# Kernel tuning notes

Hardware: AMD Instinct MI355X
Metric: run time of the kernel (lower is better)

Reference implementation:

```python
import jax, jax.numpy as jnp
import numpy as np

N = 30000   # fluid particles
E = 480000  # edges
F = 4       # fluidFeatures (in channels)
P = 8       # RBF basis size per dim (dims=[8], 1D)
LAYERS = [32, 64, 64, 2]


def hat_basis(x, n):
    # 'linear' RBF: hat functions on n evenly spaced centers in [-1, 1]
    centers = jnp.linspace(-1.0, 1.0, n, dtype=x.dtype)
    spacing = 2.0 / (n - 1)
    return jnp.maximum(0.0, 1.0 - jnp.abs(x[:, None] - centers[None, :]) / spacing)  # [E, n]


def rbf_conv(x, fi, fj, d, W, b, mask, n_nodes):
    # x: [N, Cin]; d: [E, 1] clamped; W: [P, Cin, Cout]; b: [Cout]
    phi = hat_basis(d[:, 0], W.shape[0])      # [E, P]
    xj = x[fj]                                 # gather source features [E, Cin]
    msg = jnp.zeros((xj.shape[0], W.shape[2]), dtype=x.dtype)
    for p in range(W.shape[0]):                # small fixed P=8 loop keeps memory O(E*Cout)
        msg = msg + phi[:, p, None] * (xj @ W[p])
    msg = jnp.where(mask[:, None], msg, 0.0)   # centerIgnore: drop self edges fi==fj
    out = jax.ops.segment_sum(msg, fi, num_segments=n_nodes)  # scatter-reduce to targets
    return out + b


def _xavier(key, shape_in, shape_out):
    lim = float(np.sqrt(6.0 / (shape_in + shape_out)))
    return jax.random.uniform(key, (shape_in, shape_out), jnp.float32, -lim, lim)


def setup_inputs() -> dict:
    key = jax.random.key(0)
    ks = jax.random.split(key, 16)
    fluidFeatures = jax.random.normal(ks[0], (N, F), jnp.float32)
    fi = jax.random.randint(ks[1], (E,), 0, N)
    fj = jax.random.randint(ks[2], (E,), 0, N)
    distances = jax.random.normal(ks[3], (E, 1), jnp.float32)
    # conv channels: 4->32, 64->64, 64->64, 64->2
    cio = [(F, 32), (2 * 32, 64), (64, 64), (64, 2)]
    inp = {"fluidFeatures": fluidFeatures, "fi": fi, "fj": fj, "distances": distances}
    for li, (ci, co) in enumerate(cio):
        inp[f"cW{li}"] = jax.random.normal(ks[4 + li], (P, ci, co), jnp.float32) * (1.0 / np.sqrt(P * ci))
        inp[f"cb{li}"] = jnp.zeros((co,), jnp.float32)
        inp[f"fW{li}"] = _xavier(ks[8 + li], ci, co)   # stored [in, out]
        inp[f"fb{li}"] = jnp.zeros((co,), jnp.float32)
    return inp


def reference(fluidFeatures, fi, fj, distances,
              cW0, cb0, fW0, fb0, cW1, cb1, fW1, fb1,
              cW2, cb2, fW2, fb2, cW3, cb3, fW3, fb3):
    n_nodes = fluidFeatures.shape[0]
    mask = fi != fj                     # centerIgnore (mask instead of filter: jit-safe)
    d = jnp.clip(distances, -1.0, 1.0)

    conv0 = rbf_conv(fluidFeatures, fi, fj, d, cW0, cb0, mask, n_nodes)  # [N, 32]
    lin0 = fluidFeatures @ fW0 + fb0                                      # [N, 32]
    ans = jnp.concatenate([lin0, conv0], axis=1)                          # [N, 64]

    # i = 1: features[0]=32 != features[1]=64 -> no residual
    ansc = jax.nn.relu(ans)
    ans = rbf_conv(ansc, fi, fj, d, cW1, cb1, mask, n_nodes) + (ansc @ fW1 + fb1)
    # i = 2: features[1]==features[2]==64 and shapes match -> residual
    ansc = jax.nn.relu(ans)
    ans = rbf_conv(ansc, fi, fj, d, cW2, cb2, mask, n_nodes) + (ansc @ fW2 + fb2) + ans
    # i = 3: 64 -> 2, no residual
    ansc = jax.nn.relu(ans)
    ans = rbf_conv(ansc, fi, fj, d, cW3, cb3, mask, n_nodes) + (ansc @ fW3 + fb3)

    return ans  # dim == 1 (dims=[8]) -> no /128
```

## Files before the change

kernel.cpp:

```cpp
#include <hip/hip_runtime.h>


#define CAP 48

typedef __attribute__((ext_vector_type(8))) short short8;
typedef __attribute__((ext_vector_type(4))) short short4v;
typedef __attribute__((ext_vector_type(4))) float f32x4;

__device__ __forceinline__ short bf16s(float f) {
  unsigned u = __float_as_uint(f);
  return (short)((u + 0x7FFF + ((u >> 16) & 1)) >> 16);
}
__device__ __forceinline__ float b2f(unsigned short s) {
  return __uint_as_float(((unsigned)s) << 16);
}
__device__ __forceinline__ unsigned pack2(float a, float b) {
  return (unsigned)(unsigned short)bf16s(a) | ((unsigned)(unsigned short)bf16s(b) << 16);
}

__global__ void fill_prep(const float* __restrict__ dist,
                          const int* __restrict__ fi, const int* __restrict__ fj,
                          int* __restrict__ cnt, int* __restrict__ jw, int nE,
                          const float* __restrict__ cW1, const float* __restrict__ fW1,
                          const float* __restrict__ cW2, const float* __restrict__ fW2,
                          short* __restrict__ wt1, short* __restrict__ wt2,
                          const float* __restrict__ X,
                          const float* __restrict__ cW0,
                          const float* __restrict__ fW0,
                          unsigned short* __restrict__ U0, int n,
                          int fillBlocks, int prepBlocks) {
  if ((int)blockIdx.x < fillBlocks) {
    int e = blockIdx.x * blockDim.x + threadIdx.x;
    if (e >= nE) return;
    int i = fi[e], j = fj[e];
    if (i == j) return;
    float d = fminf(1.0f, fmaxf(-1.0f, dist[e]));
    float u = (d + 1.0f) * 3.5f;
    int p = min((int)u, 6);
    float w0 = 1.0f - (u - (float)p);
    int wq = (int)(w0 * 16383.0f + 0.5f);
    int pos = atomicAdd(&cnt[i], 1);
    if (pos < CAP)
      jw[(size_t)i * CAP + pos] = j | (p << 15) | (wq << 18);
  } else if ((int)blockIdx.x < fillBlocks + prepBlocks) {
    int idx = ((int)blockIdx.x - fillBlocks) * blockDim.x + threadIdx.x;
    if (idx >= 2 * 576 * 64) return;
    int sel = idx / (576 * 64);
    int r = idx - sel * (576 * 64);
    int col = r >> 6, ch = r & 63;
    const float* cW = sel ? cW2 : cW1;
    const float* fW = sel ? fW2 : fW1;
    float v;
    if (col < 512) {
      int p = col >> 6, co = col & 63;
      v = cW[((size_t)p * 64 + ch) * 64 + co];
    } else {
      v = fW[(size_t)ch * 64 + (col - 512)];
    }
    (sel ? wt2 : wt1)[(size_t)col * 64 + ch] = bf16s(v);
  } else {
    int idx = ((int)blockIdx.x - fillBlocks - prepBlocks) * blockDim.x + threadIdx.x;
    if (idx >= n * 72) return;
    int i = idx / 72, g = idx - i * 72;
    float4 x = *(const float4*)(X + (size_t)i * 4);
    float xk[4] = {x.x, x.y, x.z, x.w};
    float s[4] = {0, 0, 0, 0};
    if (g < 64) {
      int p = g >> 3;
      int co = (g * 4) & 31;
      #pragma unroll
      for (int k = 0; k < 4; ++k) {
        const float* wr = cW0 + ((size_t)p * 4 + k) * 32 + co;
        #pragma unroll
        for (int c = 0; c < 4; ++c) s[c] = fmaf(xk[k], wr[c], s[c]);
      }
    } else {
      int co = (g - 64) * 4;
      #pragma unroll
      for (int k = 0; k < 4; ++k) {
        const float* wr = fW0 + (size_t)k * 32 + co;
        #pragma unroll
        for (int c = 0; c < 4; ++c) s[c] = fmaf(xk[k], wr[c], s[c]);
      }
    }
    uint2 pk = make_uint2(pack2(s[0], s[1]), pack2(s[2], s[3]));
    *(uint2*)(U0 + (size_t)i * 288 + g * 4) = pk;
  }
}

__device__ __forceinline__ void gemm_tail(const unsigned short* sXa, short* sUL,
                                          const short* __restrict__ WT,
                                          int w, int lane) {
  const int mrow = lane & 15;
  const int quad = lane >> 4;
  short8 b0 = *(const short8*)(sXa + mrow * 64 + quad * 8);
  short8 b1 = *(const short8*)(sXa + mrow * 64 + quad * 8 + 32);
  const short* A0 = WT + (size_t)(w * 16 + mrow) * 64 + quad * 8;
  const short* A1 = WT + (size_t)((w + 16) * 16 + mrow) * 64 + quad * 8;
  short8 a00 = *(const short8*)(A0);
  short8 a01 = *(const short8*)(A0 + 32);
  short8 a10 = *(const short8*)(A1);
  short8 a11 = *(const short8*)(A1 + 32);
  const bool has3 = (w < 4);
  short8 a20 = {0, 0, 0, 0, 0, 0, 0, 0};
  short8 a21 = {0, 0, 0, 0, 0, 0, 0, 0};
  if (has3) {
    const short* A2 = WT + (size_t)((w + 32) * 16 + mrow) * 64 + quad * 8;
    a20 = *(const short8*)(A2);
    a21 = *(const short8*)(A2 + 32);
  }
  __builtin_amdgcn_sched_barrier(0);
  f32x4 acc0 = {0, 0, 0, 0}, acc1 = {0, 0, 0, 0};
  acc0 = __builtin_amdgcn_mfma_f32_16x16x32_bf16(a00, b0, acc0, 0, 0, 0);
  acc0 = __builtin_amdgcn_mfma_f32_16x16x32_bf16(a01, b1, acc0, 0, 0, 0);
  acc1 = __builtin_amdgcn_mfma_f32_16x16x32_bf16(a10, b0, acc1, 0, 0, 0);
  acc1 = __builtin_amdgcn_mfma_f32_16x16x32_bf16(a11, b1, acc1, 0, 0, 0);
  short4v pk;
  #pragma unroll
  for (int r = 0; r < 4; ++r) pk[r] = bf16s(acc0[r]);
  *(short4v*)(sUL + mrow * 584 + w * 16 + quad * 4) = pk;
  #pragma unroll
  for (int r = 0; r < 4; ++r) pk[r] = bf16s(acc1[r]);
  *(short4v*)(sUL + mrow * 584 + (w + 16) * 16 + quad * 4) = pk;
  if (has3) {
    f32x4 acc2 = {0, 0, 0, 0};
    acc2 = __builtin_amdgcn_mfma_f32_16x16x32_bf16(a20, b0, acc2, 0, 0, 0);
    acc2 = __builtin_amdgcn_mfma_f32_16x16x32_bf16(a21, b1, acc2, 0, 0, 0);
    #pragma unroll
    for (int r = 0; r < 4; ++r) pk[r] = bf16s(acc2[r]);
    *(short4v*)(sUL + mrow * 584 + (w + 32) * 16 + quad * 4) = pk;
  }
}

__global__ __launch_bounds__(1024, 8) void layer0_gemm(
    const unsigned short* __restrict__ U0,
    const int* __restrict__ cnt, const int* __restrict__ jw,
    const float* __restrict__ cb0, const float* __restrict__ fb0,
    const short* __restrict__ WTul,
    unsigned short* __restrict__ UL, int n) {
  __shared__ __align__(16) unsigned short sXa[16 * 64];
  __shared__ __align__(16) short sUL[16 * 584];
  const int tid = threadIdx.x;
  const int w = tid >> 6;
  const int lane = tid & 63;
  const int grp = lane >> 5;
  const int gl = lane & 31;
  const int nodeBase = blockIdx.x * 16;
  const int i = nodeBase + w;
  const bool valid = (i < n);
  const int ic = valid ? i : 0;

  int rec = jw[(size_t)ic * CAP + (lane < CAP ? lane : 0)];
  const int m = valid ? min(cnt[ic], CAP) : 0;
  const int mc = m - 1;
  float accLo = 0.0f, accHi = 0.0f;
  const unsigned* __restrict__ u0W = (const unsigned*)U0;
  unsigned rA[8], rB[8];
  float wA[8], wB[8];
#define L0_LOAD(R, WS, Q0)                                                  \
  _Pragma("unroll")                                                         \
  for (int k = 0; k < 8; ++k) {                                             \
    int eA = (Q0) + 2 * k;                                                  \
    int vA = __builtin_amdgcn_readlane(rec, min(eA, mc));                   \
    int vB = __builtin_amdgcn_readlane(rec, min(eA + 1, mc));               \
    int v = grp ? vB : vA;                                                  \
    int j = v & 0x7FFF;                                                     \
    int p = (v >> 15) & 7;                                                  \
    float w0 = (float)((unsigned)v >> 18) * (1.0f / 16383.0f);              \
    float wgt = (gl < 16) ? w0 : (1.0f - w0);                               \
    WS[k] = (eA + grp < m) ? wgt : 0.0f;                                    \
    R[k] = u0W[(size_t)j * 144 + p * 16 + gl];                              \
  }
#define L0_FMA(R, WS)                                                       \
  _Pragma("unroll")                                                         \
  for (int k = 0; k < 8; ++k) {                                             \
    accLo = fmaf(WS[k], __uint_as_float(R[k] << 16), accLo);                \
    accHi = fmaf(WS[k], __uint_as_float(R[k] & 0xFFFF0000u), accHi);        \
  }
  if (m > 0) {
    L0_LOAD(rA, wA, 0);
    L0_LOAD(rB, wB, 16);
    __builtin_amdgcn_sched_barrier(0);
    L0_FMA(rA, wA);
    if (m > 16) {
      L0_FMA(rB, wB);
      for (int q0 = 32; q0 < m; q0 += 16) {
        L0_LOAD(rA, wA, q0);
        __builtin_amdgcn_sched_barrier(0);
        L0_FMA(rA, wA);
      }
    }
  }
#undef L0_LOAD
#undef L0_FMA
  accLo += __shfl_xor(accLo, 16, 64);
  accHi += __shfl_xor(accHi, 16, 64);
  accLo += __shfl_xor(accLo, 32, 64);
  accHi += __shfl_xor(accHi, 32, 64);
  if (lane < 16) {
    const int l = lane;
    float c0v = fmaxf(accLo + cb0[2 * l], 0.0f);
    float c1v = fmaxf(accHi + cb0[2 * l + 1], 0.0f);
    unsigned lr = ((const unsigned*)(U0 + (size_t)ic * 288 + 256))[l];
    float l0 = fmaxf(__uint_as_float(lr << 16) + fb0[2 * l], 0.0f);
    float l1 = fmaxf(__uint_as_float(lr & 0xFFFF0000u) + fb0[2 * l + 1], 0.0f);
    unsigned* row = (unsigned*)(sXa + w * 64);
    row[l] = pack2(l0, l1);
    row[16 + l] = pack2(c0v, c1v);
  }
  __syncthreads();

  gemm_tail(sXa, sUL, WTul, w, lane);
  __syncthreads();
  const int r = tid >> 6;
  const int c0 = tid & 63;
  if (nodeBase + r < n) {
    unsigned short* dst = UL + (size_t)(nodeBase + r) * 576;
    #pragma unroll
    for (int chunk = c0; chunk < 72; chunk += 64)
      *(short8*)(dst + chunk * 8) = *(const short8*)(sUL + r * 584 + chunk * 8);
  }
}

__global__ __launch_bounds__(1024, 8) void conv_gemm(
    const unsigned short* __restrict__ ULA,
    const int* __restrict__ cnt, const int* __restrict__ jw,
    const float* __restrict__ cb, const float* __restrict__ fb,
    const short* __restrict__ WTul2,
    float* __restrict__ outAns,
    unsigned short* __restrict__ ULB, int n) {
  __shared__ __align__(16) unsigned short sXa[16 * 64];
  __shared__ __align__(16) short sUL[16 * 584];
  const int tid = threadIdx.x;
  const int w = tid >> 6;
  const int lane = tid & 63;
  const int half = lane >> 5;
  const int pl = lane & 31;
  const int nodeBase = blockIdx.x * 16;
  const int i = nodeBase + w;
  const bool valid = (i < n);
  const int ic = valid ? i : 0;

  int rec = jw[(size_t)ic * CAP + (lane < CAP ? lane : 0)];
  const int m = valid ? min(cnt[ic], CAP) : 0;
  const int mc = m - 1;
  const unsigned Lraw = ((const unsigned*)(ULA + (size_t)ic * 576 + 512))[pl];
  float accLo = 0.0f, accHi = 0.0f;
  const unsigned* __restrict__ ulaW = (const unsigned*)ULA;
  unsigned rA[16], rB[16];
#define C1_LOAD(R, Q0)                                                      \
  _Pragma("unroll")                                                         \
  for (int k = 0; k < 16; ++k) {                                            \
    int v = __builtin_amdgcn_readlane(rec, min((Q0) + k, mc));              \
    int j = v & 0x7FFF;                                                     \
    int p = (v >> 15) & 7;                                                  \
    R[k] = ulaW[(size_t)j * 288 + p * 32 + lane];                           \
  }
#define C1_FMA(R, Q0)                                                       \
  _Pragma("unroll")                                                         \
  for (int k = 0; k < 16; ++k) {                                            \
    int v = __builtin_amdgcn_readlane(rec, min((Q0) + k, mc));              \
    float w0 = (float)((unsigned)v >> 18) * (1.0f / 16383.0f);              \
    float wv = half ? (1.0f - w0) : w0;                                     \
    wv = ((Q0) + k < m) ? wv : 0.0f;                                        \
    accLo = fmaf(wv, __uint_as_float(R[k] << 16), accLo);                   \
    accHi = fmaf(wv, __uint_as_float(R[k] & 0xFFFF0000u), accHi);           \
  }
  if (m > 0) {
    C1_LOAD(rA, 0);
    C1_LOAD(rB, 16);
    __builtin_amdgcn_sched_barrier(0);
    C1_FMA(rA, 0);
    if (m > 16) {
      C1_FMA(rB, 16);
      for (int q0 = 32; q0 < m; q0 += 16) {
        C1_LOAD(rA, q0);
        __builtin_amdgcn_sched_barrier(0);
        C1_FMA(rA, q0);
      }
    }
  }
#undef C1_LOAD
#undef C1_FMA
  accLo += __shfl_xor(accLo, 32, 64);
  accHi += __shfl_xor(accHi, 32, 64);
  if (half == 0) {
    unsigned* row = (unsigned*)(sXa + w * 64);
    if (valid) {
      const int c0i = 2 * pl, c1i = c0i + 1;
      float o0 = accLo + __uint_as_float(Lraw << 16) + cb[c0i] + fb[c0i];
      float o1 = accHi + __uint_as_float(Lraw & 0xFFFF0000u) + cb[c1i] + fb[c1i];
      *(float2*)(outAns + (size_t)i * 64 + c0i) = make_float2(o0, o1);
      row[pl] = pack2(fmaxf(o0, 0.0f), fmaxf(o1, 0.0f));
    } else {
      row[pl] = 0u;
    }
  }
  __syncthreads();

  gemm_tail(sXa, sUL, WTul2, w, lane);
  __syncthreads();
  const int r = tid >> 6;
  const int c0 = tid & 63;
  if (nodeBase + r < n) {
    unsigned short* dst = ULB + (size_t)(nodeBase + r) * 576;
    #pragma unroll
    for (int chunk = c0; chunk < 72; chunk += 64)
      *(short8*)(dst + chunk * 8) = *(const short8*)(sUL + r * 584 + chunk * 8);
  }
}

__global__ __launch_bounds__(256, 8) void conv2_kernel(
    const unsigned short* __restrict__ UL,
    const int* __restrict__ cnt, const int* __restrict__ jw,
    const float* __restrict__ cb, const float* __restrict__ fb,
    const float* __restrict__ resid,
    const float* __restrict__ cW3,
    float* __restrict__ T,
    unsigned short* __restrict__ outAnsc, int n) {
  const int lane = threadIdx.x & 63;
  const int half = lane >> 5;
  const int pl = lane & 31;
  const int i = (blockIdx.x * blockDim.x + threadIdx.x) >> 6;
  if (i >= n) return;
  int rec = jw[(size_t)i * CAP + (lane < CAP ? lane : 0)];
  const int m = min(cnt[i], CAP);
  const int mc = m - 1;
  const unsigned Lraw = ((const unsigned*)(UL + (size_t)i * 576 + 512))[pl];
  float2 rv = *(const float2*)(resid + (size_t)i * 64 + 2 * pl);
  float accLo = 0.0f, accHi = 0.0f;
  const unsigned* __restrict__ ulW = (const unsigned*)UL;
  unsigned rA[16], rB[16];
#define C2_LOAD(R, Q0)                                                      \
  _Pragma("unroll")                                                         \
  for (int k = 0; k < 16; ++k) {                                            \
    int v = __builtin_amdgcn_readlane(rec, min((Q0) + k, mc));              \
    int j = v & 0x7FFF;                                                     \
    int p = (v >> 15) & 7;                                                  \
    R[k] = ulW[(size_t)j * 288 + p * 32 + lane];                            \
  }
#define C2_FMA(R, Q0)                                                       \
  _Pragma("unroll")                                                         \
  for (int k = 0; k < 16; ++k) {                                            \
    int v = __builtin_amdgcn_readlane(rec, min((Q0) + k, mc));              \
    float w0 = (float)((unsigned)v >> 18) * (1.0f / 16383.0f);              \
    float wv = half ? (1.0f - w0) : w0;                                     \
    wv = ((Q0) + k < m) ? wv : 0.0f;                                        \
    accLo = fmaf(wv, __uint_as_float(R[k] << 16), accLo);                   \
    accHi = fmaf(wv, __uint_as_float(R[k] & 0xFFFF0000u), accHi);           \
  }
  if (m > 0) {
    C2_LOAD(rA, 0);
    C2_LOAD(rB, 16);
    __builtin_amdgcn_sched_barrier(0);
    C2_FMA(rA, 0);
    if (m > 16) {
      C2_FMA(rB, 16);
      for (int q0 = 32; q0 < m; q0 += 16) {
        C2_LOAD(rA, q0);
        __builtin_amdgcn_sched_barrier(0);
        C2_FMA(rA, q0);
      }
    }
  }
#undef C2_LOAD
#undef C2_FMA
  accLo += __shfl_xor(accLo, 32, 64);
  accHi += __shfl_xor(accHi, 32, 64);
  if (half == 0) {
    const int c0i = 2 * pl, c1i = c0i + 1;
    float o0 = accLo + __uint_as_float(Lraw << 16) + cb[c0i] + fb[c0i] + rv.x;
    float o1 = accHi + __uint_as_float(Lraw & 0xFFFF0000u) + cb[c1i] + fb[c1i] + rv.y;
    unsigned short xb0 = (unsigned short)bf16s(fmaxf(o0, 0.0f));
    unsigned short xb1 = (unsigned short)bf16s(fmaxf(o1, 0.0f));
    ((unsigned*)(outAnsc + (size_t)i * 64))[pl] = (unsigned)xb0 | ((unsigned)xb1 << 16);
    float x0 = b2f(xb0), x1 = b2f(xb1);
    float c[16];
    #pragma unroll
    for (int t = 0; t < 16; ++t) {
      const float* wrow = cW3 + ((size_t)(t >> 1) * 64) * 2 + (t & 1);
      c[t] = x0 * wrow[c0i * 2] + x1 * wrow[c1i * 2];
    }
    #pragma unroll
    for (int off = 16; off > 0; off >>= 1) {
      #pragma unroll
      for (int t = 0; t < 16; ++t) c[t] += __shfl_xor(c[t], off, 64);
    }
    if (pl == 0) {
      float* tr = T + (size_t)i * 16;
      #pragma unroll
      for (int t = 0; t < 16; ++t) tr[t] = c[t];
    }
  }
}

__global__ __launch_bounds__(256, 4) void layer3_kernel(
    const unsigned short* __restrict__ Xb,
    const float* __restrict__ T,
    const int* __restrict__ cnt, const int* __restrict__ jw,
    const float* __restrict__ cb3, const float* __restrict__ fb3,
    const float* __restrict__ fW3,
    float* __restrict__ out, int n) {
  const int lane = threadIdx.x & 63;
  const int i = (blockIdx.x * blockDim.x + threadIdx.x) >> 6;
  if (i >= n) return;
  const int m = min(cnt[i], CAP);
  float c0 = 0.0f, c1 = 0.0f;
  if (lane < m) {
    int v = jw[(size_t)i * CAP + lane];
    int j = min(v & 0x7FFF, n - 1);
    int p = (v >> 15) & 7;
    float w0 = (float)((unsigned)v >> 18) * (1.0f / 16383.0f);
    float w1 = 1.0f - w0;
    const float* tb = T + (size_t)j * 16 + p * 2;
    float2 ta = *(const float2*)(tb);
    float2 tc = *(const float2*)(tb + 2);
    c0 = w0 * ta.x + w1 * tc.x;
    c1 = w0 * ta.y + w1 * tc.y;
  }
  float xi = b2f(Xb[(size_t)i * 64 + lane]);
  float2 fw = *(const float2*)(fW3 + lane * 2);
  c0 = fmaf(xi, fw.x, c0);
  c1 = fmaf(xi, fw.y, c1);
  #pragma unroll
  for (int off = 32; off > 0; off >>= 1) {
    c0 += __shfl_xor(c0, off, 64);
    c1 += __shfl_xor(c1, off, 64);
  }
  if (lane == 0) {
    out[(size_t)i * 2 + 0] = c0 + cb3[0] + fb3[0];
    out[(size_t)i * 2 + 1] = c1 + cb3[1] + fb3[1];
  }
}

extern "C" void kernel_launch(void* const* d_in, const int* in_sizes, int n_in,
                              void* d_out, int out_size, void* d_ws, size_t ws_size,
                              hipStream_t stream) {
  const float* X    = (const float*)d_in[0];
  const int*   fi   = (const int*)d_in[1];
  const int*   fj   = (const int*)d_in[2];
  const float* dist = (const float*)d_in[3];
  const float* cW0 = (const float*)d_in[4];  const float* cb0 = (const float*)d_in[5];
  const float* fW0 = (const float*)d_in[6];  const float* fb0 = (const float*)d_in[7];
  const float* cW1 = (const float*)d_in[8];  const float* cb1 = (const float*)d_in[9];
  const float* fW1 = (const float*)d_in[10]; const float* fb1 = (const float*)d_in[11];
  const float* cW2 = (const float*)d_in[12]; const float* cb2 = (const float*)d_in[13];
  const float* fW2 = (const float*)d_in[14]; const float* fb2 = (const float*)d_in[15];
  const float* cW3 = (const float*)d_in[16]; const float* cb3 = (const float*)d_in[17];
  const float* fW3 = (const float*)d_in[18]; const float* fb3 = (const float*)d_in[19];
  float* out = (float*)d_out;

  const int n  = in_sizes[0] / 4;
  const int nE = in_sizes[1];

  unsigned short* ULA   = (unsigned short*)d_ws;
  unsigned short* ULB   = ULA + (size_t)n * 576;
  unsigned short* U0    = ULB;
  float*          ans1  = (float*)(ULB + (size_t)n * 576);
  unsigned short* ansc2 = (unsigned short*)(ans1 + (size_t)n * 64);
  float* T     = (float*)(ansc2 + (size_t)n * 64);
  short* wtul1 = (short*)(T + (size_t)n * 16);
  short* wtul2 = wtul1 + 576 * 64;
  int*   jw    = (int*)(wtul2 + 576 * 64);
  int*   cnt   = jw + (size_t)n * CAP;

  hipMemsetAsync(cnt, 0, (size_t)n * sizeof(int), stream);
  const int fillBlocks = (nE + 255) / 256;
  const int prepBlocks = (2 * 576 * 64 + 255) / 256;
  const int u0Blocks   = (n * 72 + 255) / 256;
  fill_prep<<<fillBlocks + prepBlocks + u0Blocks, 256, 0, stream>>>(
      dist, fi, fj, cnt, jw, nE, cW1, fW1, cW2, fW2, wtul1, wtul2,
      X, cW0, fW0, U0, n, fillBlocks, prepBlocks);

  layer0_gemm<<<(n + 15) / 16, 1024, 0, stream>>>(U0, cnt, jw, cb0, fb0,
                                                  wtul1, ULA, n);
  conv_gemm<<<(n + 15) / 16, 1024, 0, stream>>>(ULA, cnt, jw, cb1, fb1,
                                                wtul2, ans1, ULB, n);
  conv2_kernel<<<(n * 64 + 255) / 256, 256, 0, stream>>>(
      ULB, cnt, jw, cb2, fb2, ans1, cW3, T, ansc2, n);
  layer3_kernel<<<(n * 64 + 255) / 256, 256, 0, stream>>>(ansc2, T, cnt, jw,
                                                          cb3, fb3, fW3, out, n);
}
```

Measured before the change: 246.3 us.

## Pre-encode byte offsets and weights in edge records to drop per-edge decode and bounds masks

Edge records now store a combined source offset (j*9+p) plus a validity flag and a 12-bit weight, so the gather kernels form byte addresses with one shift, mask and add, and get the weight via a float bit trick instead of integer decode and a multiply. The whole jw table is zeroed each call, so unused slots decode to zero weight and offset 0. That removes the min() clamps on readlane indices and the per-edge validity selects. The cost is a larger memset each call, coarser weight quantization, and a T stride padded to 18 so the j*9+p offset indexes it directly.

```diff
diff --git a/kernel.cpp b/kernel.cpp
--- a/kernel.cpp
+++ b/kernel.cpp
@@ -16,6 +16,12 @@
 }
 __device__ __forceinline__ unsigned pack2(float a, float b) {
   return (unsigned)(unsigned short)bf16s(a) | ((unsigned)(unsigned short)bf16s(b) << 16);
+}
+__device__ __forceinline__ float dec_w0(int v) {
+  return __uint_as_float(0x3F800000u | (((unsigned)v & 0xFFFu) << 11)) - 1.0f;
+}
+__device__ __forceinline__ float dec_sf(int v) {
+  return (float)(((unsigned)v >> 12) & 1u);
 }
 
 __global__ void fill_prep(const float* __restrict__ dist,
@@ -38,10 +44,11 @@
     float u = (d + 1.0f) * 3.5f;
     int p = min((int)u, 6);
     float w0 = 1.0f - (u - (float)p);
-    int wq = (int)(w0 * 16383.0f + 0.5f);
+    int wq = min((int)(w0 * 4096.0f + 0.5f), 4095);
+    unsigned off = (unsigned)(j * 9 + p);
     int pos = atomicAdd(&cnt[i], 1);
     if (pos < CAP)
-      jw[(size_t)i * CAP + pos] = j | (p << 15) | (wq << 18);
+      jw[(size_t)i * CAP + pos] = (int)((off << 13) | 0x1000u | (unsigned)wq);
   } else if ((int)blockIdx.x < fillBlocks + prepBlocks) {
     int idx = ((int)blockIdx.x - fillBlocks) * blockDim.x + threadIdx.x;
     if (idx >= 2 * 576 * 64) return;
@@ -145,31 +152,28 @@
   const int lane = tid & 63;
   const int grp = lane >> 5;
   const int gl = lane & 31;
+  const unsigned gl4 = (unsigned)gl * 4u;
   const int nodeBase = blockIdx.x * 16;
   const int i = nodeBase + w;
   const bool valid = (i < n);
   const int ic = valid ? i : 0;
+  const char* __restrict__ u0B = (const char*)U0;
 
   int rec = jw[(size_t)ic * CAP + (lane < CAP ? lane : 0)];
   const int m = valid ? min(cnt[ic], CAP) : 0;
-  const int mc = m - 1;
   float accLo = 0.0f, accHi = 0.0f;
-  const unsigned* __restrict__ u0W = (const unsigned*)U0;
   unsigned rA[8], rB[8];
   float wA[8], wB[8];
 #define L0_LOAD(R, WS, Q0)                                                  \
   _Pragma("unroll")                                                         \
   for (int k = 0; k < 8; ++k) {                                             \
-    int eA = (Q0) + 2 * k;                                                  \
-    int vA = __builtin_amdgcn_readlane(rec, min(eA, mc));                   \
-    int vB = __builtin_amdgcn_readlane(rec, min(eA + 1, mc));               \
+    int vA = __builtin_amdgcn_readlane(rec, (Q0) + 2 * k);                  \
+    int vB = __builtin_amdgcn_readlane(rec, (Q0) + 2 * k + 1);              \
     int v = grp ? vB : vA;                                                  \
-    int j = v & 0x7FFF;                                                     \
-    int p = (v >> 15) & 7;                                                  \
-    float w0 = (float)((unsigned)v >> 18) * (1.0f / 16383.0f);              \
-    float wgt = (gl < 16) ? w0 : (1.0f - w0);                               \
-    WS[k] = (eA + grp < m) ? wgt : 0.0f;                                    \
-    R[k] = u0W[(size_t)j * 144 + p * 16 + gl];                              \
+    unsigned voff = (((unsigned)v >> 7) & 0xFFFFFFC0u) + gl4;               \
+    R[k] = *(const unsigned*)(u0B + voff);                                  \
+    float w0 = dec_w0(v);                                                   \
+    WS[k] = (gl < 16) ? w0 : (dec_sf(v) - w0);                              \
   }
 #define L0_FMA(R, WS)                                                       \
   _Pragma("unroll")                                                         \
@@ -236,35 +240,33 @@
   const int lane = tid & 63;
   const int half = lane >> 5;
   const int pl = lane & 31;
+  const unsigned lane4 = (unsigned)lane * 4u;
   const int nodeBase = blockIdx.x * 16;
   const int i = nodeBase + w;
   const bool valid = (i < n);
   const int ic = valid ? i : 0;
+  const char* __restrict__ ulB = (const char*)ULA;
 
   int rec = jw[(size_t)ic * CAP + (lane < CAP ? lane : 0)];
   const int m = valid ? min(cnt[ic], CAP) : 0;
-  const int mc = m - 1;
   const unsigned Lraw = ((const unsigned*)(ULA + (size_t)ic * 576 + 512))[pl];
   float accLo = 0.0f, accHi = 0.0f;
-  const unsigned* __restrict__ ulaW = (const unsigned*)ULA;
   unsigned rA[16], rB[16];
-#define C1_LOAD(R, Q0)                                                      \
-  _Pragma("unroll")                                                         \
-  for (int k = 0; k < 16; ++k) {                                            \
-    int v = __builtin_amdgcn_readlane(rec, min((Q0) + k, mc));              \
-    int j = v & 0x7FFF;                                                     \
-    int p = (v >> 15) & 7;                                                  \
-    R[k] = ulaW[(size_t)j * 288 + p * 32 + lane];                           \
-  }
-#define C1_FMA(R, Q0)                                                       \
-  _Pragma("unroll")                                                         \
-  for (int k = 0; k < 16; ++k) {                                            \
-    int v = __builtin_amdgcn_readlane(rec, min((Q0) + k, mc));              \
-    float w0 = (float)((unsigned)v >> 18) * (1.0f / 16383.0f);              \
-    float wv = half ? (1.0f - w0) : w0;                                     \
-    wv = ((Q0) + k < m) ? wv : 0.0f;                                        \
-    accLo = fmaf(wv, __uint_as_float(R[k] << 16), accLo);                   \
-    accHi = fmaf(wv, __uint_as_float(R[k] & 0xFFFF0000u), accHi);           \
+#define C1_LOAD(R, Q0)                                                     \
+  _Pragma("unroll")                                                        \
+  for (int k = 0; k < 16; ++k) {                                           \
+    int v = __builtin_amdgcn_readlane(rec, (Q0) + k);                      \
+    unsigned voff = (((unsigned)v >> 6) & 0xFFFFFF80u) + lane4;            \
+    R[k] = *(const unsigned*)(ulB + voff);                                 \
+  }
+#define C1_FMA(R, Q0)                                                      \
+  _Pragma("unroll")                                                        \
+  for (int k = 0; k < 16; ++k) {                                           \
+    int v = __builtin_amdgcn_readlane(rec, (Q0) + k);                      \
+    float w0 = dec_w0(v);                                                  \
+    float wv = half ? (dec_sf(v) - w0) : w0;                               \
+    accLo = fmaf(wv, __uint_as_float(R[k] << 16), accLo);                  \
+    accHi = fmaf(wv, __uint_as_float(R[k] & 0xFFFF0000u), accHi);          \
   }
   if (m > 0) {
     C1_LOAD(rA, 0);
@@ -321,33 +323,31 @@
   const int lane = threadIdx.x & 63;
   const int half = lane >> 5;
   const int pl = lane & 31;
+  const unsigned lane4 = (unsigned)lane * 4u;
   const int i = (blockIdx.x * blockDim.x + threadIdx.x) >> 6;
   if (i >= n) return;
+  const char* __restrict__ ulB = (const char*)UL;
   int rec = jw[(size_t)i * CAP + (lane < CAP ? lane : 0)];
   const int m = min(cnt[i], CAP);
-  const int mc = m - 1;
   const unsigned Lraw = ((const unsigned*)(UL + (size_t)i * 576 + 512))[pl];
   float2 rv = *(const float2*)(resid + (size_t)i * 64 + 2 * pl);
   float accLo = 0.0f, accHi = 0.0f;
-  const unsigned* __restrict__ ulW = (const unsigned*)UL;
   unsigned rA[16], rB[16];
-#define C2_LOAD(R, Q0)                                                      \
-  _Pragma("unroll")                                                         \
-  for (int k = 0; k < 16; ++k) {                                            \
-    int v = __builtin_amdgcn_readlane(rec, min((Q0) + k, mc));              \
-    int j = v & 0x7FFF;                                                     \
-    int p = (v >> 15) & 7;                                                  \
-    R[k] = ulW[(size_t)j * 288 + p * 32 + lane];                            \
-  }
-#define C2_FMA(R, Q0)                                                       \
-  _Pragma("unroll")                                                         \
-  for (int k = 0; k < 16; ++k) {                                            \
-    int v = __builtin_amdgcn_readlane(rec, min((Q0) + k, mc));              \
-    float w0 = (float)((unsigned)v >> 18) * (1.0f / 16383.0f);              \
-    float wv = half ? (1.0f - w0) : w0;                                     \
-    wv = ((Q0) + k < m) ? wv : 0.0f;                                        \
-    accLo = fmaf(wv, __uint_as_float(R[k] << 16), accLo);                   \
-    accHi = fmaf(wv, __uint_as_float(R[k] & 0xFFFF0000u), accHi);           \
+#define C2_LOAD(R, Q0)                                                     \
+  _Pragma("unroll")                                                        \
+  for (int k = 0; k < 16; ++k) {                                           \
+    int v = __builtin_amdgcn_readlane(rec, (Q0) + k);                      \
+    unsigned voff = (((unsigned)v >> 6) & 0xFFFFFF80u) + lane4;            \
+    R[k] = *(const unsigned*)(ulB + voff);                                 \
+  }
+#define C2_FMA(R, Q0)                                                      \
+  _Pragma("unroll")                                                        \
+  for (int k = 0; k < 16; ++k) {                                           \
+    int v = __builtin_amdgcn_readlane(rec, (Q0) + k);                      \
+    float w0 = dec_w0(v);                                                  \
+    float wv = half ? (dec_sf(v) - w0) : w0;                               \
+    accLo = fmaf(wv, __uint_as_float(R[k] << 16), accLo);                  \
+    accHi = fmaf(wv, __uint_as_float(R[k] & 0xFFFF0000u), accHi);          \
   }
   if (m > 0) {
     C2_LOAD(rA, 0);
@@ -387,7 +387,7 @@
       for (int t = 0; t < 16; ++t) c[t] += __shfl_xor(c[t], off, 64);
     }
     if (pl == 0) {
-      float* tr = T + (size_t)i * 16;
+      float* tr = T + (size_t)i * 18;
       #pragma unroll
       for (int t = 0; t < 16; ++t) tr[t] = c[t];
     }
@@ -408,11 +408,10 @@
   float c0 = 0.0f, c1 = 0.0f;
   if (lane < m) {
     int v = jw[(size_t)i * CAP + lane];
-    int j = min(v & 0x7FFF, n - 1);
-    int p = (v >> 15) & 7;
-    float w0 = (float)((unsigned)v >> 18) * (1.0f / 16383.0f);
+    unsigned off = (unsigned)v >> 13;
+    float w0 = dec_w0(v);
     float w1 = 1.0f - w0;
-    const float* tb = T + (size_t)j * 16 + p * 2;
+    const float* tb = T + (size_t)off * 2;
     float2 ta = *(const float2*)(tb);
     float2 tc = *(const float2*)(tb + 2);
     c0 = w0 * ta.x + w1 * tc.x;
@@ -459,12 +458,12 @@
   float*          ans1  = (float*)(ULB + (size_t)n * 576);
   unsigned short* ansc2 = (unsigned short*)(ans1 + (size_t)n * 64);
   float* T     = (float*)(ansc2 + (size_t)n * 64);
-  short* wtul1 = (short*)(T + (size_t)n * 16);
+  short* wtul1 = (short*)(T + (size_t)n * 18);
   short* wtul2 = wtul1 + 576 * 64;
   int*   jw    = (int*)(wtul2 + 576 * 64);
   int*   cnt   = jw + (size_t)n * CAP;
 
-  hipMemsetAsync(cnt, 0, (size_t)n * sizeof(int), stream);
+  hipMemsetAsync(jw, 0, ((size_t)n * CAP + n) * sizeof(int), stream);
   const int fillBlocks = (nE + 255) / 256;
   const int prepBlocks = (2 * 576 * 64 + 255) / 256;
   const int u0Blocks   = (n * 72 + 255) / 256;
```

New measurement: 244.0 us. Within noise of the previous version (-0.9%).
